# Kernel tuning notes

Measured on AMD Instinct MI355X. Metric: run time of the kernel, lower is better.

Reference implementation:

```python
import jax, jax.numpy as jnp
import numpy as np


def reference(x, edge_index, edge_attr, W, b):
    """PyG GCNConv: out = D^{-1/2} (A + I) D^{-1/2} X W + b.

    x: [N, Din] node features
    edge_index: [2, E] int (row=source, col=target)
    edge_attr: [E] edge weights
    W: [Din, Dout], b: [Dout]
    """
    N = x.shape[0]
    # add self-loops with weight 1 (PyG fill_value=1.0)
    loop = jnp.arange(N, dtype=edge_index.dtype)
    row = jnp.concatenate([edge_index[0], loop])
    col = jnp.concatenate([edge_index[1], loop])
    w = jnp.concatenate([edge_attr, jnp.ones((N,), dtype=edge_attr.dtype)])

    # symmetric normalization: norm_e = d[row]^-1/2 * w_e * d[col]^-1/2
    deg = jax.ops.segment_sum(w, col, num_segments=N)
    dis = jnp.where(deg > 0, jax.lax.rsqrt(jnp.where(deg > 0, deg, 1.0)), 0.0)
    norm = dis[row] * w * dis[col]

    # linear projection first (Din == Dout, cheaper either way), then
    # gather-scale-scatter aggregation at targets
    h = x @ W                                   # [N, Dout]
    msg = h[row] * norm[:, None]                # [E+N, Dout]
    out = jax.ops.segment_sum(msg, col, num_segments=N)  # [N, Dout]
    return out + b


def setup_inputs() -> dict:
    key = jax.random.key(0)
    k1, k2, k3, k4 = jax.random.split(key, 4)
    N, E, Din, Dout = 100000, 1600000, 128, 128
    x = jax.random.normal(k1, (N, Din), dtype=jnp.float32)
    edge_index = jax.random.randint(k2, (2, E), 0, N, dtype=jnp.int64)
    edge_attr = jax.random.uniform(k3, (E,), dtype=jnp.float32)
    # Glorot init like PyG Linear default
    W = jax.random.normal(k4, (Din, Dout), dtype=jnp.float32) * (1.0 / np.sqrt(Din))
    b = jnp.zeros((Dout,), dtype=jnp.float32)
    return {"x": x, "edge_index": edge_index, "edge_attr": edge_attr, "W": W, "b": b}
```

## Files before the change

### kernel.cpp

```cpp
#include <hip/hip_runtime.h>


#define ELEMS_PER_SCAN_BLOCK 2048
#define CHUNK 4096

typedef __attribute__((ext_vector_type(8))) short short8;
typedef __attribute__((ext_vector_type(4))) float f32x4;

__device__ inline unsigned short f2bf(float f) {
    unsigned u = __float_as_uint(f);
    u += 0x7fffu + ((u >> 16) & 1u);
    return (unsigned short)(u >> 16);
}
__device__ inline float bf_lo(unsigned u) { return __uint_as_float(u << 16); }
__device__ inline float bf_hi(unsigned u) { return __uint_as_float(u & 0xffff0000u); }

__global__ __launch_bounds__(256) void k_hist(const int* __restrict__ col,
                                              int* __restrict__ histg,
                                              int E, int NC, int NBLK) {
    __shared__ int lh[1024];
    int t = threadIdx.x, blk = blockIdx.x;
    for (int i = t; i < 1024; i += 256) lh[i] = 0;
    __syncthreads();
    int base = blk * CHUNK;
    #pragma unroll
    for (int i = 0; i < CHUNK / 256; ++i) {
        int e = base + i * 256 + t;
        if (e < E) atomicAdd(&lh[col[e] >> 7], 1);
    }
    __syncthreads();
    for (int b = t; b < NC; b += 256) histg[b * NBLK + blk] = lh[b];
}

__device__ inline int wave_incl_scan(int x, int lane) {
    #pragma unroll
    for (int d = 1; d < 64; d <<= 1) {
        int y = __shfl_up(x, d, 64);
        if (lane >= d) x += y;
    }
    return x;
}

__global__ void k_scan1(const int* __restrict__ in, int* __restrict__ out,
                        int* __restrict__ bsum, int M) {
    __shared__ int wsum[4];
    __shared__ int woff[4];
    int t = threadIdx.x, lane = t & 63, wid = t >> 6;
    int base = blockIdx.x * ELEMS_PER_SCAN_BLOCK + t * 8;
    int v[8];
    #pragma unroll
    for (int i = 0; i < 8; ++i) v[i] = (base + i < M) ? in[base + i] : 0;
    int run = 0;
    #pragma unroll
    for (int i = 0; i < 8; ++i) { int x = v[i]; v[i] = run; run += x; }
    int incl = wave_incl_scan(run, lane);
    int excl = incl - run;
    if (lane == 63) wsum[wid] = incl;
    __syncthreads();
    if (t == 0) {
        int r = 0;
        #pragma unroll
        for (int w = 0; w < 4; ++w) { int s = wsum[w]; woff[w] = r; r += s; }
        bsum[blockIdx.x] = r;
    }
    __syncthreads();
    int off = woff[wid] + excl;
    #pragma unroll
    for (int i = 0; i < 8; ++i)
        if (base + i < M) out[base + i] = v[i] + off;
}

__global__ void k_scan2(const int* __restrict__ bsum, int* __restrict__ boff, int NB) {
    __shared__ int wsum[4];
    __shared__ int woff[4];
    int t = threadIdx.x, lane = t & 63, wid = t >> 6;
    int x = (t < NB) ? bsum[t] : 0;
    int incl = wave_incl_scan(x, lane);
    int excl = incl - x;
    if (lane == 63) wsum[wid] = incl;
    __syncthreads();
    if (t == 0) {
        int r = 0;
        #pragma unroll
        for (int w = 0; w < 4; ++w) { int s = wsum[w]; woff[w] = r; r += s; }
    }
    __syncthreads();
    if (t < NB) boff[t] = woff[wid] + excl;
}

__global__ void k_scan3(int* __restrict__ arr, const int* __restrict__ boff, int M) {
    int t = threadIdx.x;
    int base = blockIdx.x * ELEMS_PER_SCAN_BLOCK + t * 8;
    int off = boff[blockIdx.x];
    #pragma unroll
    for (int i = 0; i < 8; ++i) {
        int idx = base + i;
        if (idx < M) arr[idx] += off;
    }
}

__global__ __launch_bounds__(256) void k_place(const int* __restrict__ row,
                                               const int* __restrict__ col,
                                               const float* __restrict__ wgt,
                                               const int* __restrict__ histg,
                                               int* __restrict__ scol,
                                               int2* __restrict__ srw,
                                               int E, int NC, int NBLK) {
    __shared__ int lo[1024];
    int t = threadIdx.x, blk = blockIdx.x;
    for (int b = t; b < NC; b += 256) lo[b] = histg[b * NBLK + blk];
    __syncthreads();
    int base = blk * CHUNK;
    #pragma unroll
    for (int i = 0; i < CHUNK / 256; ++i) {
        int e = base + i * 256 + t;
        if (e < E) {
            int c = col[e];
            int pos = atomicAdd(&lo[c >> 7], 1);
            scol[pos] = c;
            srw[pos] = make_int2(row[e], __float_as_int(wgt[e]));
        }
    }
}

__global__ __launch_bounds__(256) void k_fine(const int* __restrict__ histg,
                                              const int* __restrict__ scol,
                                              const int2* __restrict__ srw,
                                              int* __restrict__ rowptr,
                                              float* __restrict__ dis,
                                              int2* __restrict__ spack,
                                              int E, int N, int NC, int NBLK) {
    __shared__ int cnt128[128];
    __shared__ float degf[128];
    __shared__ int cur128[128];
    __shared__ int wtot[2];
    int t = threadIdx.x, b = blockIdx.x;
    int nb = b << 7;
    int start = histg[b * NBLK];
    int end = (b == NC - 1) ? E : histg[(b + 1) * NBLK];
    if (t < 128) { cnt128[t] = 0; degf[t] = 1.0f; }
    __syncthreads();
    for (int j = start + t; j < end; j += 256) {
        int c = scol[j] - nb;
        atomicAdd(&cnt128[c], 1);
        atomicAdd(&degf[c], __int_as_float(srw[j].y));
    }
    __syncthreads();
    int v = 0, incl = 0;
    if (t < 128) {
        v = cnt128[t];
        incl = wave_incl_scan(v, t & 63);
        if ((t & 63) == 63) wtot[t >> 6] = incl;
    }
    __syncthreads();
    if (t < 128) {
        int excl = incl - v + ((t >= 64) ? wtot[0] : 0);
        int p = start + excl;
        cur128[t] = p;
        int n = nb + t;
        if (n < N) {
            rowptr[n] = p;
            dis[n] = rsqrtf(degf[t]);
        }
    }
    if (t == 0 && b == NC - 1) rowptr[N] = E;
    __syncthreads();
    for (int j = start + t; j < end; j += 256) {
        int c = scol[j] - nb;
        int pos = atomicAdd(&cur128[c], 1);
        spack[pos] = srw[j];
    }
}

__global__ void k_wprep(const float* __restrict__ W, unsigned short* __restrict__ Wtg) {
    int n = blockIdx.x;
    int k = threadIdx.x;
    Wtg[n * 128 + k] = f2bf(W[k * 128 + n]);
}

__global__ __launch_bounds__(256) void k_gemm(const float* __restrict__ x,
                                              const unsigned short* __restrict__ Wtg,
                                              unsigned short* __restrict__ h, int N) {
    __shared__ short Xs[64][136];
    __shared__ short Ws[128][136];
    int t = threadIdx.x;
    int lane = t & 63, wid = t >> 6;
    int row0 = blockIdx.x * 64;
    {
        int r = t >> 2;
        int kseg = (t & 3) * 32;
        int gr = row0 + r;
        const float4* src = (const float4*)(x + (size_t)gr * 128 + kseg);
        #pragma unroll
        for (int i = 0; i < 4; ++i) {
            float4 v0 = make_float4(0.f, 0.f, 0.f, 0.f), v1 = v0;
            if (gr < N) { v0 = src[2 * i]; v1 = src[2 * i + 1]; }
            short8 p;
            p[0] = (short)f2bf(v0.x); p[1] = (short)f2bf(v0.y);
            p[2] = (short)f2bf(v0.z); p[3] = (short)f2bf(v0.w);
            p[4] = (short)f2bf(v1.x); p[5] = (short)f2bf(v1.y);
            p[6] = (short)f2bf(v1.z); p[7] = (short)f2bf(v1.w);
            *(short8*)&Xs[r][kseg + 8 * i] = p;
        }
    }
    {
        int n = t >> 1;
        int seg = (t & 1) * 64;
        const short* wsrc = (const short*)Wtg + n * 128 + seg;
        #pragma unroll
        for (int i = 0; i < 8; ++i)
            *(short8*)&Ws[n][seg + 8 * i] = *(const short8*)(wsrc + 8 * i);
    }
    __syncthreads();

    int q = lane >> 4;
    int m = lane & 15;
    f32x4 acc[8];
    #pragma unroll
    for (int tde = 0; tde < 8; ++tde) acc[tde] = (f32x4){0.f, 0.f, 0.f, 0.f};
    #pragma unroll
    for (int kc = 0; kc < 128; kc += 32) {
        short8 af = *(const short8*)&Xs[wid * 16 + m][kc + q * 8];
        #pragma unroll
        for (int tde = 0; tde < 8; ++tde) {
            short8 bf = *(const short8*)&Ws[tde * 16 + m][kc + q * 8];
            acc[tde] = __builtin_amdgcn_mfma_f32_16x16x32_bf16(af, bf, acc[tde], 0, 0, 0);
        }
    }
    #pragma unroll
    for (int r = 0; r < 4; ++r) {
        int grow = row0 + wid * 16 + q * 4 + r;
        if (grow < N) {
            #pragma unroll
            for (int tde = 0; tde < 8; ++tde)
                h[(size_t)grow * 128 + tde * 16 + m] = f2bf(acc[tde][r]);
        }
    }
}

__global__ __launch_bounds__(256) void k_gather(const uint2* __restrict__ hb2,
                                                const float* __restrict__ dis,
                                                const int* __restrict__ rowptr,
                                                const int2* __restrict__ spack,
                                                const float* __restrict__ bias,
                                                float* __restrict__ out, int N) {
    int gid = blockIdx.x * blockDim.x + threadIdx.x;
    int node = gid >> 6;
    int lane = gid & 63;
    if (node >= N) return;
    node = __builtin_amdgcn_readfirstlane(node);
    int half = lane >> 5, sub = lane & 31;

    float dn = dis[node];
    float4 acc = make_float4(0.f, 0.f, 0.f, 0.f);
    {
        uint2 us = hb2[(size_t)node * 32 + sub];
        float s = (half == 0) ? dn : 0.0f;
        acc.x = s * bf_lo(us.x); acc.y = s * bf_hi(us.x);
        acc.z = s * bf_lo(us.y); acc.w = s * bf_hi(us.y);
    }
    int jb = rowptr[node], je = rowptr[node + 1];
    int j = jb;
    for (; j + 8 <= je; j += 8) {
        int2 p0 = spack[j + half];
        int2 p1 = spack[j + 2 + half];
        int2 p2 = spack[j + 4 + half];
        int2 p3 = spack[j + 6 + half];
        uint2 h0 = hb2[(size_t)p0.x * 32 + sub];
        uint2 h1 = hb2[(size_t)p1.x * 32 + sub];
        uint2 h2 = hb2[(size_t)p2.x * 32 + sub];
        uint2 h3 = hb2[(size_t)p3.x * 32 + sub];
        float a0 = dis[p0.x] * __int_as_float(p0.y);
        float a1 = dis[p1.x] * __int_as_float(p1.y);
        float a2 = dis[p2.x] * __int_as_float(p2.y);
        float a3 = dis[p3.x] * __int_as_float(p3.y);
        acc.x = fmaf(a0, bf_lo(h0.x), acc.x); acc.y = fmaf(a0, bf_hi(h0.x), acc.y);
        acc.z = fmaf(a0, bf_lo(h0.y), acc.z); acc.w = fmaf(a0, bf_hi(h0.y), acc.w);
        acc.x = fmaf(a1, bf_lo(h1.x), acc.x); acc.y = fmaf(a1, bf_hi(h1.x), acc.y);
        acc.z = fmaf(a1, bf_lo(h1.y), acc.z); acc.w = fmaf(a1, bf_hi(h1.y), acc.w);
        acc.x = fmaf(a2, bf_lo(h2.x), acc.x); acc.y = fmaf(a2, bf_hi(h2.x), acc.y);
        acc.z = fmaf(a2, bf_lo(h2.y), acc.z); acc.w = fmaf(a2, bf_hi(h2.y), acc.w);
        acc.x = fmaf(a3, bf_lo(h3.x), acc.x); acc.y = fmaf(a3, bf_hi(h3.x), acc.y);
        acc.z = fmaf(a3, bf_lo(h3.y), acc.z); acc.w = fmaf(a3, bf_hi(h3.y), acc.w);
    }
    for (; j < je; j += 2) {
        int e = j + half;
        bool act = e < je;
        int2 p = act ? spack[e] : make_int2(0, 0);
        uint2 hh = hb2[(size_t)(act ? p.x : 0) * 32 + sub];
        float a = act ? dis[p.x] * __int_as_float(p.y) : 0.0f;
        acc.x = fmaf(a, bf_lo(hh.x), acc.x); acc.y = fmaf(a, bf_hi(hh.x), acc.y);
        acc.z = fmaf(a, bf_lo(hh.y), acc.z); acc.w = fmaf(a, bf_hi(hh.y), acc.w);
    }
    acc.x += __shfl_xor(acc.x, 32);
    acc.y += __shfl_xor(acc.y, 32);
    acc.z += __shfl_xor(acc.z, 32);
    acc.w += __shfl_xor(acc.w, 32);
    if (half == 0) {
        float4 bv = ((const float4*)bias)[sub];
        float4 o = make_float4(bv.x + dn * acc.x, bv.y + dn * acc.y,
                               bv.z + dn * acc.z, bv.w + dn * acc.w);
        ((float4*)(out + (size_t)node * 128))[sub] = o;
    }
}

extern "C" void kernel_launch(void* const* d_in, const int* in_sizes, int n_in,
                              void* d_out, int out_size, void* d_ws, size_t ws_size,
                              hipStream_t stream) {
    const float* x     = (const float*)d_in[0];
    const int*   eidx  = (const int*)d_in[1];
    const float* eattr = (const float*)d_in[2];
    const float* W     = (const float*)d_in[3];
    const float* bias  = (const float*)d_in[4];
    int N = in_sizes[0] / 128;
    int E = in_sizes[2];
    const int* row = eidx;
    const int* col = eidx + E;

    int NC = (N + 127) >> 7;
    int NBLK = (E + CHUNK - 1) / CHUNK;

    char* p = (char*)d_ws;
    auto carve = [&](size_t bytes) {
        char* q = p;
        p += (bytes + 255) & ~(size_t)255;
        return q;
    };
    unsigned short* h   = (unsigned short*)carve((size_t)N * 128 * sizeof(unsigned short));
    unsigned short* Wtg = (unsigned short*)carve(128 * 128 * sizeof(unsigned short));
    float* dis    = (float*)carve((size_t)N * sizeof(float));
    int*   rowptr = (int*)carve((size_t)(N + 1) * sizeof(int));
    int*   histg  = (int*)carve((size_t)NC * NBLK * sizeof(int));
    int*   scol   = (int*)carve((size_t)E * sizeof(int));
    int2*  srw    = (int2*)carve((size_t)E * sizeof(int2));
    int2*  spack  = (int2*)carve((size_t)E * sizeof(int2));
    int*   bsum   = (int*)carve(256 * sizeof(int));
    int*   boff   = (int*)carve(256 * sizeof(int));

    int M = NC * NBLK;
    int NBs = (M + ELEMS_PER_SCAN_BLOCK - 1) / ELEMS_PER_SCAN_BLOCK;

    k_hist<<<NBLK, 256, 0, stream>>>(col, histg, E, NC, NBLK);
    k_scan1<<<NBs, 256, 0, stream>>>(histg, histg, bsum, M);
    k_scan2<<<1, 256, 0, stream>>>(bsum, boff, NBs);
    k_scan3<<<NBs, 256, 0, stream>>>(histg, boff, M);
    k_place<<<NBLK, 256, 0, stream>>>(row, col, eattr, histg, scol, srw, E, NC, NBLK);
    k_fine<<<NC, 256, 0, stream>>>(histg, scol, srw, rowptr, dis, spack, E, N, NC, NBLK);
    k_wprep<<<128, 128, 0, stream>>>(W, Wtg);
    k_gemm<<<(N + 63) / 64, 256, 0, stream>>>(x, Wtg, h, N);
    {
        size_t threads = (size_t)N * 64;
        int blocks = (int)((threads + 255) / 256);
        k_gather<<<blocks, 256, 0, stream>>>((const uint2*)h, dis, rowptr, spack,
                                             bias, (float*)d_out, N);
    }
}
```

Measured before the change: 292.5 us.

## Pack local column into row index and gather one edge per wave

Encodes the 7-bit local target column into the upper bits of the source-row field so the separate scol array is no longer written and reread during the sort. The gather kernel is changed so that each wave handles one edge at a time across all 64 lanes (two features per lane). Edge metadata is read with wave-uniform loads and the cross-half shuffle reduction is dropped. This relies on node indices fitting in 17 bits, and it changes per-load width and memory-level parallelism in the gather.

```diff
diff --git a/kernel.cpp b/kernel.cpp
--- a/kernel.cpp
+++ b/kernel.cpp
@@ -103,7 +103,6 @@
                                                const int* __restrict__ col,
                                                const float* __restrict__ wgt,
                                                const int* __restrict__ histg,
-                                               int* __restrict__ scol,
                                                int2* __restrict__ srw,
                                                int E, int NC, int NBLK) {
     __shared__ int lo[1024];
@@ -117,14 +116,12 @@
         if (e < E) {
             int c = col[e];
             int pos = atomicAdd(&lo[c >> 7], 1);
-            scol[pos] = c;
-            srw[pos] = make_int2(row[e], __float_as_int(wgt[e]));
+            srw[pos] = make_int2(((c & 127) << 17) | row[e], __float_as_int(wgt[e]));
         }
     }
 }
 
 __global__ __launch_bounds__(256) void k_fine(const int* __restrict__ histg,
-                                              const int* __restrict__ scol,
                                               const int2* __restrict__ srw,
                                               int* __restrict__ rowptr,
                                               float* __restrict__ dis,
@@ -141,9 +138,10 @@
     if (t < 128) { cnt128[t] = 0; degf[t] = 1.0f; }
     __syncthreads();
     for (int j = start + t; j < end; j += 256) {
-        int c = scol[j] - nb;
+        int2 s = srw[j];
+        int c = s.x >> 17;
         atomicAdd(&cnt128[c], 1);
-        atomicAdd(&degf[c], __int_as_float(srw[j].y));
+        atomicAdd(&degf[c], __int_as_float(s.y));
     }
     __syncthreads();
     int v = 0, incl = 0;
@@ -166,9 +164,10 @@
     if (t == 0 && b == NC - 1) rowptr[N] = E;
     __syncthreads();
     for (int j = start + t; j < end; j += 256) {
-        int c = scol[j] - nb;
+        int2 s = srw[j];
+        int c = s.x >> 17;
         int pos = atomicAdd(&cur128[c], 1);
-        spack[pos] = srw[j];
+        spack[pos] = make_int2(s.x & 0x1FFFF, s.y);
     }
 }
 
@@ -238,10 +237,10 @@
     }
 }
 
-__global__ __launch_bounds__(256) void k_gather(const uint2* __restrict__ hb2,
+__global__ __launch_bounds__(256) void k_gather(const unsigned int* __restrict__ hb,
                                                 const float* __restrict__ dis,
                                                 const int* __restrict__ rowptr,
-                                                const int2* __restrict__ spack,
+                                                const long* __restrict__ spackl,
                                                 const float* __restrict__ bias,
                                                 float* __restrict__ out, int N) {
     int gid = blockIdx.x * blockDim.x + threadIdx.x;
@@ -249,59 +248,74 @@
     int lane = gid & 63;
     if (node >= N) return;
     node = __builtin_amdgcn_readfirstlane(node);
-    int half = lane >> 5, sub = lane & 31;
 
     float dn = dis[node];
-    float4 acc = make_float4(0.f, 0.f, 0.f, 0.f);
-    {
-        uint2 us = hb2[(size_t)node * 32 + sub];
-        float s = (half == 0) ? dn : 0.0f;
-        acc.x = s * bf_lo(us.x); acc.y = s * bf_hi(us.x);
-        acc.z = s * bf_lo(us.y); acc.w = s * bf_hi(us.y);
-    }
+    unsigned u = hb[(size_t)node * 64 + lane];
+    float2 acc;
+    acc.x = dn * bf_lo(u);
+    acc.y = dn * bf_hi(u);
+
     int jb = rowptr[node], je = rowptr[node + 1];
     int j = jb;
     for (; j + 8 <= je; j += 8) {
-        int2 p0 = spack[j + half];
-        int2 p1 = spack[j + 2 + half];
-        int2 p2 = spack[j + 4 + half];
-        int2 p3 = spack[j + 6 + half];
-        uint2 h0 = hb2[(size_t)p0.x * 32 + sub];
-        uint2 h1 = hb2[(size_t)p1.x * 32 + sub];
-        uint2 h2 = hb2[(size_t)p2.x * 32 + sub];
-        uint2 h3 = hb2[(size_t)p3.x * 32 + sub];
-        float a0 = dis[p0.x] * __int_as_float(p0.y);
-        float a1 = dis[p1.x] * __int_as_float(p1.y);
-        float a2 = dis[p2.x] * __int_as_float(p2.y);
-        float a3 = dis[p3.x] * __int_as_float(p3.y);
-        acc.x = fmaf(a0, bf_lo(h0.x), acc.x); acc.y = fmaf(a0, bf_hi(h0.x), acc.y);
-        acc.z = fmaf(a0, bf_lo(h0.y), acc.z); acc.w = fmaf(a0, bf_hi(h0.y), acc.w);
-        acc.x = fmaf(a1, bf_lo(h1.x), acc.x); acc.y = fmaf(a1, bf_hi(h1.x), acc.y);
-        acc.z = fmaf(a1, bf_lo(h1.y), acc.z); acc.w = fmaf(a1, bf_hi(h1.y), acc.w);
-        acc.x = fmaf(a2, bf_lo(h2.x), acc.x); acc.y = fmaf(a2, bf_hi(h2.x), acc.y);
-        acc.z = fmaf(a2, bf_lo(h2.y), acc.z); acc.w = fmaf(a2, bf_hi(h2.y), acc.w);
-        acc.x = fmaf(a3, bf_lo(h3.x), acc.x); acc.y = fmaf(a3, bf_hi(h3.x), acc.y);
-        acc.z = fmaf(a3, bf_lo(h3.y), acc.z); acc.w = fmaf(a3, bf_hi(h3.y), acc.w);
-    }
-    for (; j < je; j += 2) {
-        int e = j + half;
-        bool act = e < je;
-        int2 p = act ? spack[e] : make_int2(0, 0);
-        uint2 hh = hb2[(size_t)(act ? p.x : 0) * 32 + sub];
-        float a = act ? dis[p.x] * __int_as_float(p.y) : 0.0f;
-        acc.x = fmaf(a, bf_lo(hh.x), acc.x); acc.y = fmaf(a, bf_hi(hh.x), acc.y);
-        acc.z = fmaf(a, bf_lo(hh.y), acc.z); acc.w = fmaf(a, bf_hi(hh.y), acc.w);
-    }
-    acc.x += __shfl_xor(acc.x, 32);
-    acc.y += __shfl_xor(acc.y, 32);
-    acc.z += __shfl_xor(acc.z, 32);
-    acc.w += __shfl_xor(acc.w, 32);
-    if (half == 0) {
-        float4 bv = ((const float4*)bias)[sub];
-        float4 o = make_float4(bv.x + dn * acc.x, bv.y + dn * acc.y,
-                               bv.z + dn * acc.z, bv.w + dn * acc.w);
-        ((float4*)(out + (size_t)node * 128))[sub] = o;
-    }
+        long q0 = __builtin_nontemporal_load(spackl + j);
+        long q1 = __builtin_nontemporal_load(spackl + j + 1);
+        long q2 = __builtin_nontemporal_load(spackl + j + 2);
+        long q3 = __builtin_nontemporal_load(spackl + j + 3);
+        long q4 = __builtin_nontemporal_load(spackl + j + 4);
+        long q5 = __builtin_nontemporal_load(spackl + j + 5);
+        long q6 = __builtin_nontemporal_load(spackl + j + 6);
+        long q7 = __builtin_nontemporal_load(spackl + j + 7);
+        int r0 = __builtin_amdgcn_readfirstlane((int)q0);
+        int r1 = __builtin_amdgcn_readfirstlane((int)q1);
+        int r2 = __builtin_amdgcn_readfirstlane((int)q2);
+        int r3 = __builtin_amdgcn_readfirstlane((int)q3);
+        int r4 = __builtin_amdgcn_readfirstlane((int)q4);
+        int r5 = __builtin_amdgcn_readfirstlane((int)q5);
+        int r6 = __builtin_amdgcn_readfirstlane((int)q6);
+        int r7 = __builtin_amdgcn_readfirstlane((int)q7);
+        unsigned u0 = hb[(size_t)r0 * 64 + lane];
+        unsigned u1 = hb[(size_t)r1 * 64 + lane];
+        unsigned u2 = hb[(size_t)r2 * 64 + lane];
+        unsigned u3 = hb[(size_t)r3 * 64 + lane];
+        unsigned u4 = hb[(size_t)r4 * 64 + lane];
+        unsigned u5 = hb[(size_t)r5 * 64 + lane];
+        unsigned u6 = hb[(size_t)r6 * 64 + lane];
+        unsigned u7 = hb[(size_t)r7 * 64 + lane];
+        float a0 = dis[r0] * __uint_as_float((unsigned)(q0 >> 32));
+        float a1 = dis[r1] * __uint_as_float((unsigned)(q1 >> 32));
+        float a2 = dis[r2] * __uint_as_float((unsigned)(q2 >> 32));
+        float a3 = dis[r3] * __uint_as_float((unsigned)(q3 >> 32));
+        float a4 = dis[r4] * __uint_as_float((unsigned)(q4 >> 32));
+        float a5 = dis[r5] * __uint_as_float((unsigned)(q5 >> 32));
+        float a6 = dis[r6] * __uint_as_float((unsigned)(q6 >> 32));
+        float a7 = dis[r7] * __uint_as_float((unsigned)(q7 >> 32));
+        acc.x = fmaf(a0, bf_lo(u0), acc.x); acc.y = fmaf(a0, bf_hi(u0), acc.y);
+        acc.x = fmaf(a1, bf_lo(u1), acc.x); acc.y = fmaf(a1, bf_hi(u1), acc.y);
+        acc.x = fmaf(a2, bf_lo(u2), acc.x); acc.y = fmaf(a2, bf_hi(u2), acc.y);
+        acc.x = fmaf(a3, bf_lo(u3), acc.x); acc.y = fmaf(a3, bf_hi(u3), acc.y);
+        acc.x = fmaf(a4, bf_lo(u4), acc.x); acc.y = fmaf(a4, bf_hi(u4), acc.y);
+        acc.x = fmaf(a5, bf_lo(u5), acc.x); acc.y = fmaf(a5, bf_hi(u5), acc.y);
+        acc.x = fmaf(a6, bf_lo(u6), acc.x); acc.y = fmaf(a6, bf_hi(u6), acc.y);
+        acc.x = fmaf(a7, bf_lo(u7), acc.x); acc.y = fmaf(a7, bf_hi(u7), acc.y);
+    }
+    for (; j < je; ++j) {
+        long q = __builtin_nontemporal_load(spackl + j);
+        int r = __builtin_amdgcn_readfirstlane((int)q);
+        unsigned uu = hb[(size_t)r * 64 + lane];
+        float a = dis[r] * __uint_as_float((unsigned)(q >> 32));
+        acc.x = fmaf(a, bf_lo(uu), acc.x);
+        acc.y = fmaf(a, bf_hi(uu), acc.y);
+    }
+
+    int c0 = lane * 2;
+    float2 bv = *(const float2*)(bias + c0);
+    float2 o;
+    o.x = bv.x + dn * acc.x;
+    o.y = bv.y + dn * acc.y;
+    union { float2 f; double d; } cvt;
+    cvt.f = o;
+    __builtin_nontemporal_store(cvt.d, (double*)(out + (size_t)node * 128 + c0));
 }
 
 extern "C" void kernel_launch(void* const* d_in, const int* in_sizes, int n_in,
@@ -331,7 +345,6 @@
     float* dis    = (float*)carve((size_t)N * sizeof(float));
     int*   rowptr = (int*)carve((size_t)(N + 1) * sizeof(int));
     int*   histg  = (int*)carve((size_t)NC * NBLK * sizeof(int));
-    int*   scol   = (int*)carve((size_t)E * sizeof(int));
     int2*  srw    = (int2*)carve((size_t)E * sizeof(int2));
     int2*  spack  = (int2*)carve((size_t)E * sizeof(int2));
     int*   bsum   = (int*)carve(256 * sizeof(int));
@@ -344,14 +357,14 @@
     k_scan1<<<NBs, 256, 0, stream>>>(histg, histg, bsum, M);
     k_scan2<<<1, 256, 0, stream>>>(bsum, boff, NBs);
     k_scan3<<<NBs, 256, 0, stream>>>(histg, boff, M);
-    k_place<<<NBLK, 256, 0, stream>>>(row, col, eattr, histg, scol, srw, E, NC, NBLK);
-    k_fine<<<NC, 256, 0, stream>>>(histg, scol, srw, rowptr, dis, spack, E, N, NC, NBLK);
+    k_place<<<NBLK, 256, 0, stream>>>(row, col, eattr, histg, srw, E, NC, NBLK);
+    k_fine<<<NC, 256, 0, stream>>>(histg, srw, rowptr, dis, spack, E, N, NC, NBLK);
     k_wprep<<<128, 128, 0, stream>>>(W, Wtg);
     k_gemm<<<(N + 63) / 64, 256, 0, stream>>>(x, Wtg, h, N);
     {
         size_t threads = (size_t)N * 64;
         int blocks = (int)((threads + 255) / 256);
-        k_gather<<<blocks, 256, 0, stream>>>((const uint2*)h, dis, rowptr, spack,
-                                             bias, (float*)d_out, N);
-    }
-}
+        k_gather<<<blocks, 256, 0, stream>>>((const unsigned int*)h, dis, rowptr,
+                                             (const long*)spack, bias, (float*)d_out, N);
+    }
+}
```

After: 277.1 us. 1.06x faster.
